# Kernel optimization log

Hardware: AMD Instinct MI355X
Metric: run time of the kernel (lower is better)

The kernel has to match this reference:

```python
import jax, jax.numpy as jnp
import numpy as np

N = 50000
E = 800000
NODE_CONT = 64
EDGE_CAT = 16
HID = 96
LAT = 64
NUM_LAYERS = 2
BN_EPS = 1e-5


def setup_inputs() -> dict:
    key = jax.random.key(0)
    ks = jax.random.split(key, 24)
    s = 0.05
    inp = {
        "x_cont": jax.random.normal(ks[0], (N, NODE_CONT), jnp.float32),
        "x_cat": jax.random.randint(ks[1], (N,), 0, 1),
        "edge_index": jax.random.randint(ks[2], (2, E), 0, N),
        "edge_attr_cat": jax.random.randint(ks[3], (E,), 0, EDGE_CAT),
        "edge_attr_cont": jax.random.normal(ks[4], (E, 1), jnp.float32),
        # parameters
        "w_node": jax.random.normal(ks[5], (HID, NODE_CONT), jnp.float32) * s,
        "b_node": jnp.zeros((HID,), jnp.float32),
        "edge_embed": jax.random.normal(ks[6], (EDGE_CAT, HID), jnp.float32) * s,
        "gcn_w": jax.random.normal(ks[7], (NUM_LAYERS, HID, HID), jnp.float32) * s,
        "gcn_b": jnp.zeros((NUM_LAYERS, HID), jnp.float32),
        "bn_gamma": jnp.ones((NUM_LAYERS, HID), jnp.float32),
        "bn_beta": jnp.zeros((NUM_LAYERS, HID), jnp.float32),
        "mlp_w1": jax.random.normal(ks[8], (NUM_LAYERS, HID, 2 * HID), jnp.float32) * s,
        "mlp_b1": jnp.zeros((NUM_LAYERS, HID), jnp.float32),
        "mlp_w2": jax.random.normal(ks[9], (NUM_LAYERS, HID, HID), jnp.float32) * s,
        "mlp_b2": jnp.zeros((NUM_LAYERS, HID), jnp.float32),
        "mu_w": jax.random.normal(ks[10], (LAT, HID), jnp.float32) * s,
        "mu_b": jnp.zeros((LAT,), jnp.float32),
        "lv_w": jax.random.normal(ks[11], (LAT, HID), jnp.float32) * s,
        "lv_b": jnp.zeros((LAT,), jnp.float32),
    }
    return inp


def _forward(x_cont, edge_index, edge_attr_cat,
             w_node, b_node, edge_embed,
             gcn_w, gcn_b, bn_gamma, bn_beta,
             mlp_w1, mlp_b1, mlp_w2, mlp_b2,
             mu_w, mu_b, lv_w, lv_b):
    n = x_cont.shape[0]
    # node embed (only continuous path active)
    h = x_cont @ w_node.T + b_node                      # [N, H]
    # edge embed (only categorical path active) -- memory-bound gather
    edge_h = edge_embed[edge_attr_cat]                  # [E, H]
    src, dst = edge_index[0], edge_index[1]
    # GCNConv: add self-loops, symmetric normalization
    loop = jnp.arange(n)
    src_f = jnp.concatenate([src, loop])
    dst_f = jnp.concatenate([dst, loop])
    deg = jax.ops.segment_sum(jnp.ones_like(dst_f, jnp.float32), dst_f, num_segments=n)
    dinv = jax.lax.rsqrt(deg)                           # deg >= 1 (self loops)
    norm = (dinv[src_f] * dinv[dst_f])[:, None]         # [E+N, 1]
    # edge_pooled: O(E) segment-mean replacing the O(N*E) python loop;
    # edge_h is constant across layers so compute it once.
    cnt = jax.ops.segment_sum(jnp.ones((edge_h.shape[0],), edge_h.dtype), dst, num_segments=n)
    pooled = jax.ops.segment_sum(edge_h, dst, num_segments=n) / jnp.maximum(cnt, 1.0)[:, None]
    for l in range(gcn_w.shape[0]):
        msg = (h @ gcn_w[l].T)[src_f] * norm            # gather + scale
        h_gnn = jax.ops.segment_sum(msg, dst_f, num_segments=n) + gcn_b[l]
        hc = jnp.concatenate([h_gnn, pooled], axis=-1)  # [N, 2H]
        h = jax.nn.relu(hc @ mlp_w1[l].T + mlp_b1[l]) @ mlp_w2[l].T + mlp_b2[l]
        # BatchNorm1d (training-mode batch stats, biased variance)
        mean = jnp.mean(h, axis=0)
        var = jnp.mean((h - mean) ** 2, axis=0)
        h = (h - mean) * jax.lax.rsqrt(var + BN_EPS) * bn_gamma[l] + bn_beta[l]
        h = jax.nn.relu(h)
        # dropout: eval mode (identity)
    mu = h @ mu_w.T + mu_b
    logvar = h @ lv_w.T + lv_b
    return mu, logvar


def reference(x_cont, x_cat, edge_index, edge_attr_cat, edge_attr_cont,
              w_node, b_node, edge_embed, gcn_w, gcn_b, bn_gamma, bn_beta,
              mlp_w1, mlp_b1, mlp_w2, mlp_b2, mu_w, mu_b, lv_w, lv_b):
    # x_cat and edge_attr_cont are unused: in_node_cat_dim=0, in_edge_cont_dim=0
    return _forward(x_cont, edge_index, edge_attr_cat,
                    w_node, b_node, edge_embed,
                    gcn_w, gcn_b, bn_gamma, bn_beta,
                    mlp_w1, mlp_b1, mlp_w2, mlp_b2,
                    mu_w, mu_b, lv_w, lv_b)
```

## Files before the change

kernel.cpp:

```cpp
#include <hip/hip_runtime.h>

#define N_NODES 50000
#define N_EDGES 800000
#define HID 96
#define NODE_CONT 64
#define LATD 64
#define EDGE_CATN 16
#define BN_EPS 1e-5f
#define CPAD 16
#define BCAP 48
#define MLP_BLOCKS 625

typedef __attribute__((ext_vector_type(8))) short bf16x8;
typedef __attribute__((ext_vector_type(4))) float f32x4;

__device__ __forceinline__ unsigned short f2bf(float f) {
    union { float f; unsigned u; } c; c.f = f;
    unsigned r = (c.u + 0x7fffu + ((c.u >> 16) & 1u)) >> 16;
    return (unsigned short)r;
}
__device__ __forceinline__ float bf2f(unsigned short u) {
    union { unsigned u; float f; } c; c.u = ((unsigned)u) << 16;
    return c.f;
}

__global__ void k_build(const int* __restrict__ ei, const int* __restrict__ ecat,
                        int* __restrict__ cnt, int* __restrict__ csr) {
    int e = blockIdx.x * blockDim.x + threadIdx.x;
    if (e >= N_EDGES) return;
    int dst = ei[N_EDGES + e];
    int r = atomicAdd(&cnt[dst * CPAD], 1);
    if (r < BCAP) csr[dst * BCAP + r] = (ei[e] << 4) | (ecat[e] & 15);
}

__global__ void k_dinv(const int* __restrict__ cnt, float* __restrict__ dinv) {
    int n = blockIdx.x * blockDim.x + threadIdx.x;
    if (n >= N_NODES) return;
    dinv[n] = rsqrtf((float)(cnt[n * CPAD] + 1));
}

template<int POOL>
__global__ __launch_bounds__(256) void k_aggregate(
    const int* __restrict__ csr, const int* __restrict__ cnt,
    const unsigned short* __restrict__ bt, const float* __restrict__ dinv,
    const float* __restrict__ gcn_b, unsigned short* __restrict__ bg,
    const float* __restrict__ eemb, unsigned short* __restrict__ bp)
{
    __shared__ float s_eemb[EDGE_CATN * HID];
    if constexpr (POOL) {
        for (int i = threadIdx.x; i < EDGE_CATN * HID; i += 256)
            s_eemb[i] = eemb[i];
        __syncthreads();
    }
    int node = blockIdx.x * 8 + (threadIdx.x >> 5);
    int lane = threadIdx.x & 31;
    if (node >= N_NODES) return;
    float dd = dinv[node];
    const unsigned short* tn = bt + (size_t)node * HID;
    float a0 = bf2f(tn[lane]);
    float a1 = bf2f(tn[lane + 32]);
    float a2 = bf2f(tn[lane + 64]);
    float p0 = 0.f, p1 = 0.f, p2 = 0.f;
    int deg = cnt[node * CPAD];
    if (deg > BCAP) deg = BCAP;
    int beg = node * BCAP, end = beg + deg;
    int p = beg;
    for (; p + 4 <= end; p += 4) {
        int e0 = csr[p], e1 = csr[p + 1], e2 = csr[p + 2], e3 = csr[p + 3];
        const unsigned short* r0 = bt + (size_t)(e0 >> 4) * HID;
        const unsigned short* r1 = bt + (size_t)(e1 >> 4) * HID;
        const unsigned short* r2 = bt + (size_t)(e2 >> 4) * HID;
        const unsigned short* r3 = bt + (size_t)(e3 >> 4) * HID;
        unsigned short v00 = r0[lane], v01 = r0[lane + 32], v02 = r0[lane + 64];
        unsigned short v10 = r1[lane], v11 = r1[lane + 32], v12 = r1[lane + 64];
        unsigned short v20 = r2[lane], v21 = r2[lane + 32], v22 = r2[lane + 64];
        unsigned short v30 = r3[lane], v31 = r3[lane + 32], v32 = r3[lane + 64];
        a0 += (bf2f(v00) + bf2f(v10)) + (bf2f(v20) + bf2f(v30));
        a1 += (bf2f(v01) + bf2f(v11)) + (bf2f(v21) + bf2f(v31));
        a2 += (bf2f(v02) + bf2f(v12)) + (bf2f(v22) + bf2f(v32));
        if constexpr (POOL) {
            const float* q0 = s_eemb + (e0 & 15) * HID;
            const float* q1 = s_eemb + (e1 & 15) * HID;
            const float* q2 = s_eemb + (e2 & 15) * HID;
            const float* q3 = s_eemb + (e3 & 15) * HID;
            p0 += (q0[lane] + q1[lane]) + (q2[lane] + q3[lane]);
            p1 += (q0[lane + 32] + q1[lane + 32]) + (q2[lane + 32] + q3[lane + 32]);
            p2 += (q0[lane + 64] + q1[lane + 64]) + (q2[lane + 64] + q3[lane + 64]);
        }
    }
    for (; p < end; ++p) {
        int e0 = csr[p];
        const unsigned short* r = bt + (size_t)(e0 >> 4) * HID;
        a0 += bf2f(r[lane]);
        a1 += bf2f(r[lane + 32]);
        a2 += bf2f(r[lane + 64]);
        if constexpr (POOL) {
            const float* q = s_eemb + (e0 & 15) * HID;
            p0 += q[lane]; p1 += q[lane + 32]; p2 += q[lane + 64];
        }
    }
    unsigned short* o = bg + (size_t)node * HID;
    o[lane]      = f2bf(a0 * dd + gcn_b[lane]);
    o[lane + 32] = f2bf(a1 * dd + gcn_b[lane + 32]);
    o[lane + 64] = f2bf(a2 * dd + gcn_b[lane + 64]);
    if constexpr (POOL) {
        float inv = 1.f / (float)(deg < 1 ? 1 : deg);
        unsigned short* ob = bp + (size_t)node * HID;
        ob[lane]      = f2bf(p0 * inv);
        ob[lane + 32] = f2bf(p1 * inv);
        ob[lane + 64] = f2bf(p2 * inv);
    }
}

#define OFF_WNODE 0
#define OFF_GCN   6144
#define OFF_W1    24576
#define OFF_W2    61440
#define OFF_MU    79872
#define OFF_LV    86016
#define W_TOTAL   92160

__global__ void k_wprep(const float* __restrict__ w_node, const float* __restrict__ gcn_w,
                        const float* __restrict__ w1, const float* __restrict__ w2,
                        const float* __restrict__ mu_w, const float* __restrict__ lv_w,
                        const float* __restrict__ b_node,
                        unsigned short* __restrict__ out, float* __restrict__ fused_b) {
    int i = blockIdx.x * blockDim.x + threadIdx.x;
    if (i < HID * NODE_CONT) {
        int j = i / NODE_CONT, k = i - j * NODE_CONT;
        float s = 0.f;
#pragma unroll 8
        for (int q = 0; q < HID; ++q) s += gcn_w[j * HID + q] * w_node[q * NODE_CONT + k];
        out[OFF_WNODE + i] = f2bf(s);
        if (k == 0) {
            float sb = 0.f;
#pragma unroll 8
            for (int q = 0; q < HID; ++q) sb += gcn_w[j * HID + q] * b_node[q];
            fused_b[j] = sb;
        }
    } else if (i < W_TOTAL) {
        float v;
        if (i < OFF_W1)       v = gcn_w[i - OFF_GCN];
        else if (i < OFF_W2)  v = w1[i - OFF_W1];
        else if (i < OFF_MU)  v = w2[i - OFF_W2];
        else if (i < OFF_LV)  v = mu_w[i - OFF_MU];
        else                  v = lv_w[i - OFF_LV];
        out[i] = f2bf(v);
    }
}

template<int NJT, int AF32, int K1, int K2>
__global__ __launch_bounds__(320) void k_gemm_bf(
    const void* __restrict__ A1v,
    const unsigned short* __restrict__ A2,
    const float* __restrict__ ss,
    const unsigned short* __restrict__ Wb,
    const float* __restrict__ bias, const float* __restrict__ bias2,
    const float* __restrict__ rowscale,
    unsigned short* __restrict__ Yb, float* __restrict__ Yf, float* __restrict__ Yf2,
    int act)
{
    constexpr int K = K1 + K2;
    const int tile = blockIdx.x * 5 + (threadIdx.x >> 6);
    const int lane = threadIdx.x & 63;
    const int m = lane & 15;
    const int kg = lane >> 4;

    f32x4 acc[NJT];
#pragma unroll
    for (int jt = 0; jt < NJT; ++jt) acc[jt] = (f32x4){0.f, 0.f, 0.f, 0.f};

    const int arow = tile * 16 + m;

#pragma unroll
    for (int k0 = 0; k0 < K; k0 += 32) {
        int gk = k0 + kg * 8;
        bf16x8 a;
        if constexpr (AF32) {
            const float* apf = (const float*)A1v + (size_t)arow * K1 + gk;
            float4 x0 = *reinterpret_cast<const float4*>(apf);
            float4 x1 = *reinterpret_cast<const float4*>(apf + 4);
            a[0] = f2bf(x0.x); a[1] = f2bf(x0.y); a[2] = f2bf(x0.z); a[3] = f2bf(x0.w);
            a[4] = f2bf(x1.x); a[5] = f2bf(x1.y); a[6] = f2bf(x1.z); a[7] = f2bf(x1.w);
        } else {
            const unsigned short* A1 = (const unsigned short*)A1v;
            const unsigned short* ap = (gk < K1) ? A1 + (size_t)arow * K1 + gk
                                                 : A2 + (size_t)arow * K2 + (gk - K1);
            a = *reinterpret_cast<const bf16x8*>(ap);
            if (ss) {
#pragma unroll
                for (int i = 0; i < 8; ++i) {
                    float v = bf2f((unsigned short)a[i]);
                    v = fmaxf(v * ss[gk + i] + ss[96 + gk + i], 0.f);
                    a[i] = (short)f2bf(v);
                }
            }
        }
#pragma unroll
        for (int jt = 0; jt < NJT; ++jt) {
            const unsigned short* wp = Wb + (size_t)(jt * 16 + m) * K + gk;
            bf16x8 b = *reinterpret_cast<const bf16x8*>(wp);
            acc[jt] = __builtin_amdgcn_mfma_f32_16x16x32_bf16(a, b, acc[jt], 0, 0, 0);
        }
    }

    const int crow = tile * 16 + kg * 4;
    float rs[4] = {1.f, 1.f, 1.f, 1.f};
    if (rowscale) {
#pragma unroll
        for (int r = 0; r < 4; ++r) rs[r] = rowscale[crow + r];
    }
#pragma unroll
    for (int jt = 0; jt < NJT; ++jt) {
        int j = jt * 16 + m;
        float bv = 0.f;
        if (Yf2) bv = (jt < NJT / 2) ? bias[j] : bias2[j - (NJT / 2) * 16];
        else if (bias) bv = bias[j];
#pragma unroll
        for (int r = 0; r < 4; ++r) {
            float v = acc[jt][r] + bv;
            if (act) v = fmaxf(v, 0.f);
            v *= rs[r];
            int row = crow + r;
            if (Yf2) {
                if (jt < NJT / 2) Yf[(size_t)row * ((NJT / 2) * 16) + j] = v;
                else              Yf2[(size_t)row * ((NJT / 2) * 16) + (j - (NJT / 2) * 16)] = v;
            } else {
                Yb[(size_t)row * (NJT * 16) + j] = f2bf(v);
            }
        }
    }
}

__global__ __launch_bounds__(320) void k_mlp(
    const unsigned short* __restrict__ A1, const unsigned short* __restrict__ A2,
    const unsigned short* __restrict__ W1, const float* __restrict__ b1,
    const unsigned short* __restrict__ W2, const float* __restrict__ b2,
    unsigned short* __restrict__ bh, float* __restrict__ partials)
{
    __shared__ float s_stat[192];
    __shared__ unsigned short s_z1[5][16][104];
    for (int j = threadIdx.x; j < 192; j += 320) s_stat[j] = 0.f;
    const int wid = threadIdx.x >> 6;
    const int tile = blockIdx.x * 5 + wid;
    const int lane = threadIdx.x & 63;
    const int m = lane & 15;
    const int kg = lane >> 4;
    const int arow = tile * 16 + m;

    f32x4 acc[6];
#pragma unroll
    for (int jt = 0; jt < 6; ++jt) acc[jt] = (f32x4){0.f, 0.f, 0.f, 0.f};

#pragma unroll
    for (int k0 = 0; k0 < 192; k0 += 32) {
        int gk = k0 + kg * 8;
        const unsigned short* ap = (gk < 96) ? A1 + (size_t)arow * 96 + gk
                                             : A2 + (size_t)arow * 96 + (gk - 96);
        bf16x8 a = *reinterpret_cast<const bf16x8*>(ap);
#pragma unroll
        for (int jt = 0; jt < 6; ++jt) {
            bf16x8 b = *reinterpret_cast<const bf16x8*>(W1 + (size_t)(jt * 16 + m) * 192 + gk);
            acc[jt] = __builtin_amdgcn_mfma_f32_16x16x32_bf16(a, b, acc[jt], 0, 0, 0);
        }
    }
#pragma unroll
    for (int jt = 0; jt < 6; ++jt) {
        int j = jt * 16 + m;
        float bv = b1[j];
#pragma unroll
        for (int r = 0; r < 4; ++r)
            s_z1[wid][kg * 4 + r][j] = f2bf(fmaxf(acc[jt][r] + bv, 0.f));
    }
    __syncthreads();

    f32x4 acc2[6];
#pragma unroll
    for (int jt = 0; jt < 6; ++jt) acc2[jt] = (f32x4){0.f, 0.f, 0.f, 0.f};
#pragma unroll
    for (int k0 = 0; k0 < 96; k0 += 32) {
        int gk = k0 + kg * 8;
        bf16x8 a = *reinterpret_cast<const bf16x8*>(&s_z1[wid][m][gk]);
#pragma unroll
        for (int jt = 0; jt < 6; ++jt) {
            bf16x8 b = *reinterpret_cast<const bf16x8*>(W2 + (size_t)(jt * 16 + m) * 96 + gk);
            acc2[jt] = __builtin_amdgcn_mfma_f32_16x16x32_bf16(a, b, acc2[jt], 0, 0, 0);
        }
    }
    const int crow = tile * 16 + kg * 4;
#pragma unroll
    for (int jt = 0; jt < 6; ++jt) {
        int j = jt * 16 + m;
        float bv = b2[j];
        float lsum = 0.f, lsq = 0.f;
#pragma unroll
        for (int r = 0; r < 4; ++r) {
            float v = acc2[jt][r] + bv;
            lsum += v; lsq += v * v;
            bh[(size_t)(crow + r) * HID + j] = f2bf(v);
        }
        atomicAdd(&s_stat[j], lsum);
        atomicAdd(&s_stat[96 + j], lsq);
    }
    __syncthreads();
    float* prow = partials + (size_t)blockIdx.x * 192;
    for (int j = threadIdx.x; j < 192; j += 320) prow[j] = s_stat[j];
}

__global__ __launch_bounds__(64) void k_bn_reduce(
    const float* __restrict__ partials,
    const float* __restrict__ g, const float* __restrict__ b,
    float* __restrict__ ss)
{
    int j = blockIdx.x;
    int t = threadIdx.x;
    float s = 0.f, s2 = 0.f;
    for (int i = t; i < MLP_BLOCKS; i += 64) {
        s  += partials[(size_t)i * 192 + j];
        s2 += partials[(size_t)i * 192 + 96 + j];
    }
#pragma unroll
    for (int off = 32; off > 0; off >>= 1) {
        s  += __shfl_down(s, off, 64);
        s2 += __shfl_down(s2, off, 64);
    }
    if (t == 0) {
        float mean = s / (float)N_NODES;
        float var = s2 / (float)N_NODES - mean * mean;
        float sc = g[j] * rsqrtf(var + BN_EPS);
        ss[j] = sc;
        ss[96 + j] = b[j] - mean * sc;
    }
}

extern "C" void kernel_launch(void* const* d_in, const int* in_sizes, int n_in,
                              void* d_out, int out_size, void* d_ws, size_t ws_size,
                              hipStream_t stream) {
    const float* x_cont = (const float*)d_in[0];
    const int* edge_index = (const int*)d_in[2];
    const int* ecat = (const int*)d_in[3];
    const float* w_node = (const float*)d_in[5];
    const float* b_node = (const float*)d_in[6];
    const float* eemb = (const float*)d_in[7];
    const float* gcn_w = (const float*)d_in[8];
    const float* gcn_b = (const float*)d_in[9];
    const float* bn_g = (const float*)d_in[10];
    const float* bn_b = (const float*)d_in[11];
    const float* w1 = (const float*)d_in[12];
    const float* b1 = (const float*)d_in[13];
    const float* w2 = (const float*)d_in[14];
    const float* b2 = (const float*)d_in[15];
    const float* mu_w = (const float*)d_in[16];
    const float* mu_b = (const float*)d_in[17];
    const float* lv_w = (const float*)d_in[18];
    const float* lv_b = (const float*)d_in[19];
    float* out = (float*)d_out;

    char* base = (char*)d_ws;
    float* dinv     = (float*)base;                     base += (size_t)N_NODES * 4;
    float* partials = (float*)base;                     base += (size_t)MLP_BLOCKS * 192 * 4;
    float* ssbuf    = (float*)base;                     base += 2 * 192 * 4;
    float* fused_b  = (float*)base;                     base += 128 * 4;
    int*   cnt      = (int*)base;                       base += (size_t)N_NODES * CPAD * 4;
    int*   csr      = (int*)base;                       base += (size_t)N_NODES * BCAP * 4;
    unsigned short* wbf = (unsigned short*)base;        base += (size_t)W_TOTAL * 2;
    unsigned short* bh  = (unsigned short*)base;        base += (size_t)N_NODES * HID * 2;
    unsigned short* bt  = (unsigned short*)base;        base += (size_t)N_NODES * HID * 2;
    unsigned short* bg  = (unsigned short*)base;        base += (size_t)N_NODES * HID * 2;
    unsigned short* bp  = (unsigned short*)base;        base += (size_t)N_NODES * HID * 2;

    hipMemsetAsync(cnt, 0, (size_t)N_NODES * CPAD * sizeof(int), stream);

    k_wprep<<<(W_TOTAL + 255) / 256, 256, 0, stream>>>(w_node, gcn_w, w1, w2, mu_w, lv_w,
                                                       b_node, wbf, fused_b);
    k_build<<<(N_EDGES + 255) / 256, 256, 0, stream>>>(edge_index, ecat, cnt, csr);
    k_dinv<<<(N_NODES + 255) / 256, 256, 0, stream>>>(cnt, dinv);

    const int GG = N_NODES / 16 / 5;

    for (int l = 0; l < 2; ++l) {
        if (l == 0)
            k_gemm_bf<6, 1, NODE_CONT, 0><<<GG, 320, 0, stream>>>(
                x_cont, nullptr, nullptr, wbf + OFF_WNODE, fused_b, nullptr, dinv,
                bt, nullptr, nullptr, 0);
        else
            k_gemm_bf<6, 0, HID, 0><<<GG, 320, 0, stream>>>(
                bh, nullptr, ssbuf, wbf + OFF_GCN + l * HID * HID,
                nullptr, nullptr, dinv, bt, nullptr, nullptr, 0);
        if (l == 0)
            k_aggregate<1><<<N_NODES / 8, 256, 0, stream>>>(
                csr, cnt, bt, dinv, gcn_b + l * HID, bg, eemb, bp);
        else
            k_aggregate<0><<<N_NODES / 8, 256, 0, stream>>>(
                csr, cnt, bt, dinv, gcn_b + l * HID, bg, eemb, bp);
        k_mlp<<<GG, 320, 0, stream>>>(bg, bp,
                                      wbf + OFF_W1 + l * HID * 2 * HID, b1 + l * HID,
                                      wbf + OFF_W2 + l * HID * HID, b2 + l * HID,
                                      bh, partials);
        k_bn_reduce<<<96, 64, 0, stream>>>(partials, bn_g + l * HID, bn_b + l * HID,
                                           ssbuf + l * 192);
    }

    k_gemm_bf<8, 0, HID, 0><<<GG, 320, 0, stream>>>(
        bh, nullptr, ssbuf + 192, wbf + OFF_MU, mu_b, lv_b, nullptr,
        nullptr, out, out + (size_t)N_NODES * LATD, 0);
}
```

Measured before the change: 251.6 us.

## Partition CSR build by destination range with shared-memory counters, drop memset and dinv

```diff
diff --git a/kernel.cpp b/kernel.cpp
--- a/kernel.cpp
+++ b/kernel.cpp
@@ -7,9 +7,11 @@
 #define LATD 64
 #define EDGE_CATN 16
 #define BN_EPS 1e-5f
-#define CPAD 16
 #define BCAP 48
 #define MLP_BLOCKS 625
+#define PPITCH 640
+#define BUILD_BLOCKS 200
+#define NODES_PER_BLK 250
 
 typedef __attribute__((ext_vector_type(8))) short bf16x8;
 typedef __attribute__((ext_vector_type(4))) float f32x4;
@@ -24,27 +26,39 @@
     return c.f;
 }
 
-__global__ void k_build(const int* __restrict__ ei, const int* __restrict__ ecat,
-                        int* __restrict__ cnt, int* __restrict__ csr) {
-    int e = blockIdx.x * blockDim.x + threadIdx.x;
-    if (e >= N_EDGES) return;
-    int dst = ei[N_EDGES + e];
-    int r = atomicAdd(&cnt[dst * CPAD], 1);
-    if (r < BCAP) csr[dst * BCAP + r] = (ei[e] << 4) | (ecat[e] & 15);
-}
-
-__global__ void k_dinv(const int* __restrict__ cnt, float* __restrict__ dinv) {
-    int n = blockIdx.x * blockDim.x + threadIdx.x;
-    if (n >= N_NODES) return;
-    dinv[n] = rsqrtf((float)(cnt[n * CPAD] + 1));
+__global__ __launch_bounds__(512) void k_build(
+    const int* __restrict__ ei, const int* __restrict__ ecat,
+    int* __restrict__ cnt, int* __restrict__ csr)
+{
+    __shared__ int lcnt[NODES_PER_BLK];
+    const int lo = blockIdx.x * NODES_PER_BLK;
+    for (int i = threadIdx.x; i < NODES_PER_BLK; i += 512) lcnt[i] = 0;
+    __syncthreads();
+    const int4* dst4 = (const int4*)(ei + N_EDGES);
+    for (int q = threadIdx.x; q < N_EDGES / 4; q += 512) {
+        int4 d4 = dst4[q];
+        int dd[4] = {d4.x, d4.y, d4.z, d4.w};
+        int e = q * 4;
+#pragma unroll
+        for (int k = 0; k < 4; ++k) {
+            int dst = dd[k];
+            if (dst >= lo && dst < lo + NODES_PER_BLK) {
+                int r = atomicAdd(&lcnt[dst - lo], 1);
+                if (r < BCAP)
+                    csr[(size_t)dst * BCAP + r] = (ei[e + k] << 4) | (ecat[e + k] & 15);
+            }
+        }
+    }
+    __syncthreads();
+    for (int i = threadIdx.x; i < NODES_PER_BLK; i += 512) cnt[lo + i] = lcnt[i];
 }
 
 template<int POOL>
 __global__ __launch_bounds__(256) void k_aggregate(
     const int* __restrict__ csr, const int* __restrict__ cnt,
-    const unsigned short* __restrict__ bt, const float* __restrict__ dinv,
-    const float* __restrict__ gcn_b, unsigned short* __restrict__ bg,
-    const float* __restrict__ eemb, unsigned short* __restrict__ bp)
+    const unsigned short* __restrict__ bt,
+    const float* __restrict__ gcn_b, unsigned short* __restrict__ bgp,
+    const float* __restrict__ eemb)
 {
     __shared__ float s_eemb[EDGE_CATN * HID];
     if constexpr (POOL) {
@@ -55,14 +69,14 @@
     int node = blockIdx.x * 8 + (threadIdx.x >> 5);
     int lane = threadIdx.x & 31;
     if (node >= N_NODES) return;
-    float dd = dinv[node];
+    int degr = cnt[node];
+    float dd = rsqrtf((float)(degr + 1));
+    int deg = degr > BCAP ? BCAP : degr;
     const unsigned short* tn = bt + (size_t)node * HID;
     float a0 = bf2f(tn[lane]);
     float a1 = bf2f(tn[lane + 32]);
     float a2 = bf2f(tn[lane + 64]);
     float p0 = 0.f, p1 = 0.f, p2 = 0.f;
-    int deg = cnt[node * CPAD];
-    if (deg > BCAP) deg = BCAP;
     int beg = node * BCAP, end = beg + deg;
     int p = beg;
     for (; p + 4 <= end; p += 4) {
@@ -99,13 +113,13 @@
             p0 += q[lane]; p1 += q[lane + 32]; p2 += q[lane + 64];
         }
     }
-    unsigned short* o = bg + (size_t)node * HID;
+    unsigned short* o = bgp + (size_t)node * 192;
     o[lane]      = f2bf(a0 * dd + gcn_b[lane]);
     o[lane + 32] = f2bf(a1 * dd + gcn_b[lane + 32]);
     o[lane + 64] = f2bf(a2 * dd + gcn_b[lane + 64]);
     if constexpr (POOL) {
         float inv = 1.f / (float)(deg < 1 ? 1 : deg);
-        unsigned short* ob = bp + (size_t)node * HID;
+        unsigned short* ob = o + 96;
         ob[lane]      = f2bf(p0 * inv);
         ob[lane + 32] = f2bf(p1 * inv);
         ob[lane + 64] = f2bf(p2 * inv);
@@ -149,18 +163,17 @@
     }
 }
 
-template<int NJT, int AF32, int K1, int K2>
+template<int NJT, int AF32, int K1>
 __global__ __launch_bounds__(320) void k_gemm_bf(
     const void* __restrict__ A1v,
-    const unsigned short* __restrict__ A2,
     const float* __restrict__ ss,
     const unsigned short* __restrict__ Wb,
     const float* __restrict__ bias, const float* __restrict__ bias2,
-    const float* __restrict__ rowscale,
+    const int* __restrict__ cntp,
     unsigned short* __restrict__ Yb, float* __restrict__ Yf, float* __restrict__ Yf2,
     int act)
 {
-    constexpr int K = K1 + K2;
+    constexpr int K = K1;
     const int tile = blockIdx.x * 5 + (threadIdx.x >> 6);
     const int lane = threadIdx.x & 63;
     const int m = lane & 15;
@@ -183,9 +196,7 @@
             a[0] = f2bf(x0.x); a[1] = f2bf(x0.y); a[2] = f2bf(x0.z); a[3] = f2bf(x0.w);
             a[4] = f2bf(x1.x); a[5] = f2bf(x1.y); a[6] = f2bf(x1.z); a[7] = f2bf(x1.w);
         } else {
-            const unsigned short* A1 = (const unsigned short*)A1v;
-            const unsigned short* ap = (gk < K1) ? A1 + (size_t)arow * K1 + gk
-                                                 : A2 + (size_t)arow * K2 + (gk - K1);
+            const unsigned short* ap = (const unsigned short*)A1v + (size_t)arow * K1 + gk;
             a = *reinterpret_cast<const bf16x8*>(ap);
             if (ss) {
 #pragma unroll
@@ -206,9 +217,9 @@
 
     const int crow = tile * 16 + kg * 4;
     float rs[4] = {1.f, 1.f, 1.f, 1.f};
-    if (rowscale) {
-#pragma unroll
-        for (int r = 0; r < 4; ++r) rs[r] = rowscale[crow + r];
+    if (cntp) {
+#pragma unroll
+        for (int r = 0; r < 4; ++r) rs[r] = rsqrtf((float)(cntp[crow + r] + 1));
     }
 #pragma unroll
     for (int jt = 0; jt < NJT; ++jt) {
@@ -233,7 +244,7 @@
 }
 
 __global__ __launch_bounds__(320) void k_mlp(
-    const unsigned short* __restrict__ A1, const unsigned short* __restrict__ A2,
+    const unsigned short* __restrict__ A,
     const unsigned short* __restrict__ W1, const float* __restrict__ b1,
     const unsigned short* __restrict__ W2, const float* __restrict__ b2,
     unsigned short* __restrict__ bh, float* __restrict__ partials)
@@ -252,15 +263,13 @@
 #pragma unroll
     for (int jt = 0; jt < 6; ++jt) acc[jt] = (f32x4){0.f, 0.f, 0.f, 0.f};
 
+    const unsigned short* ap = A + (size_t)arow * 192 + kg * 8;
 #pragma unroll
     for (int k0 = 0; k0 < 192; k0 += 32) {
-        int gk = k0 + kg * 8;
-        const unsigned short* ap = (gk < 96) ? A1 + (size_t)arow * 96 + gk
-                                             : A2 + (size_t)arow * 96 + (gk - 96);
-        bf16x8 a = *reinterpret_cast<const bf16x8*>(ap);
+        bf16x8 a = *reinterpret_cast<const bf16x8*>(ap + k0);
 #pragma unroll
         for (int jt = 0; jt < 6; ++jt) {
-            bf16x8 b = *reinterpret_cast<const bf16x8*>(W1 + (size_t)(jt * 16 + m) * 192 + gk);
+            bf16x8 b = *reinterpret_cast<const bf16x8*>(W1 + (size_t)(jt * 16 + m) * 192 + kg * 8 + k0);
             acc[jt] = __builtin_amdgcn_mfma_f32_16x16x32_bf16(a, b, acc[jt], 0, 0, 0);
         }
     }
@@ -303,8 +312,8 @@
         atomicAdd(&s_stat[96 + j], lsq);
     }
     __syncthreads();
-    float* prow = partials + (size_t)blockIdx.x * 192;
-    for (int j = threadIdx.x; j < 192; j += 320) prow[j] = s_stat[j];
+    for (int j = threadIdx.x; j < 192; j += 320)
+        partials[(size_t)j * PPITCH + blockIdx.x] = s_stat[j];
 }
 
 __global__ __launch_bounds__(64) void k_bn_reduce(
@@ -316,8 +325,8 @@
     int t = threadIdx.x;
     float s = 0.f, s2 = 0.f;
     for (int i = t; i < MLP_BLOCKS; i += 64) {
-        s  += partials[(size_t)i * 192 + j];
-        s2 += partials[(size_t)i * 192 + 96 + j];
+        s  += partials[(size_t)j * PPITCH + i];
+        s2 += partials[(size_t)(96 + j) * PPITCH + i];
     }
 #pragma unroll
     for (int off = 32; off > 0; off >>= 1) {
@@ -357,43 +366,38 @@
     float* out = (float*)d_out;
 
     char* base = (char*)d_ws;
-    float* dinv     = (float*)base;                     base += (size_t)N_NODES * 4;
-    float* partials = (float*)base;                     base += (size_t)MLP_BLOCKS * 192 * 4;
+    float* partials = (float*)base;                     base += (size_t)192 * PPITCH * 4;
     float* ssbuf    = (float*)base;                     base += 2 * 192 * 4;
     float* fused_b  = (float*)base;                     base += 128 * 4;
-    int*   cnt      = (int*)base;                       base += (size_t)N_NODES * CPAD * 4;
+    int*   cnt      = (int*)base;                       base += (size_t)N_NODES * 4;
     int*   csr      = (int*)base;                       base += (size_t)N_NODES * BCAP * 4;
     unsigned short* wbf = (unsigned short*)base;        base += (size_t)W_TOTAL * 2;
     unsigned short* bh  = (unsigned short*)base;        base += (size_t)N_NODES * HID * 2;
     unsigned short* bt  = (unsigned short*)base;        base += (size_t)N_NODES * HID * 2;
-    unsigned short* bg  = (unsigned short*)base;        base += (size_t)N_NODES * HID * 2;
-    unsigned short* bp  = (unsigned short*)base;        base += (size_t)N_NODES * HID * 2;
-
-    hipMemsetAsync(cnt, 0, (size_t)N_NODES * CPAD * sizeof(int), stream);
+    unsigned short* bgp = (unsigned short*)base;        base += (size_t)N_NODES * 192 * 2;
 
     k_wprep<<<(W_TOTAL + 255) / 256, 256, 0, stream>>>(w_node, gcn_w, w1, w2, mu_w, lv_w,
                                                        b_node, wbf, fused_b);
-    k_build<<<(N_EDGES + 255) / 256, 256, 0, stream>>>(edge_index, ecat, cnt, csr);
-    k_dinv<<<(N_NODES + 255) / 256, 256, 0, stream>>>(cnt, dinv);
+    k_build<<<BUILD_BLOCKS, 512, 0, stream>>>(edge_index, ecat, cnt, csr);
 
     const int GG = N_NODES / 16 / 5;
 
     for (int l = 0; l < 2; ++l) {
         if (l == 0)
-            k_gemm_bf<6, 1, NODE_CONT, 0><<<GG, 320, 0, stream>>>(
-                x_cont, nullptr, nullptr, wbf + OFF_WNODE, fused_b, nullptr, dinv,
+            k_gemm_bf<6, 1, NODE_CONT><<<GG, 320, 0, stream>>>(
+                x_cont, nullptr, wbf + OFF_WNODE, fused_b, nullptr, cnt,
                 bt, nullptr, nullptr, 0);
         else
-            k_gemm_bf<6, 0, HID, 0><<<GG, 320, 0, stream>>>(
-                bh, nullptr, ssbuf, wbf + OFF_GCN + l * HID * HID,
-                nullptr, nullptr, dinv, bt, nullptr, nullptr, 0);
+            k_gemm_bf<6, 0, HID><<<GG, 320, 0, stream>>>(
+                bh, ssbuf, wbf + OFF_GCN + l * HID * HID,
+                nullptr, nullptr, cnt, bt, nullptr, nullptr, 0);
         if (l == 0)
             k_aggregate<1><<<N_NODES / 8, 256, 0, stream>>>(
-                csr, cnt, bt, dinv, gcn_b + l * HID, bg, eemb, bp);
+                csr, cnt, bt, gcn_b + l * HID, bgp, eemb);
         else
             k_aggregate<0><<<N_NODES / 8, 256, 0, stream>>>(
-                csr, cnt, bt, dinv, gcn_b + l * HID, bg, eemb, bp);
-        k_mlp<<<GG, 320, 0, stream>>>(bg, bp,
+                csr, cnt, bt, gcn_b + l * HID, bgp, eemb);
+        k_mlp<<<GG, 320, 0, stream>>>(bgp,
                                       wbf + OFF_W1 + l * HID * 2 * HID, b1 + l * HID,
                                       wbf + OFF_W2 + l * HID * HID, b2 + l * HID,
                                       bh, partials);
@@ -401,7 +405,7 @@
                                            ssbuf + l * 192);
     }
 
-    k_gemm_bf<8, 0, HID, 0><<<GG, 320, 0, stream>>>(
-        bh, nullptr, ssbuf + 192, wbf + OFF_MU, mu_b, lv_b, nullptr,
+    k_gemm_bf<8, 0, HID><<<GG, 320, 0, stream>>>(
+        bh, ssbuf + 192, wbf + OFF_MU, mu_b, lv_b, nullptr,
         nullptr, out, out + (size_t)N_NODES * LATD, 0);
 }
```

Result: slower. 444.9 us (+76.8%).
